# Performance work log

Measured on AMD Instinct MI355X. Metric: run time of the kernel, lower is better.

The kernel has to match this reference:

```python
import jax, jax.numpy as jnp
import numpy as np

N = 20000   # atoms
E = 320000  # edges (avg degree 16)
H = 128     # hidden_channels / num_filters
G = 128     # num_gaussians
L = 4       # num_interactions
B = 200     # molecules
V = 80      # _MAX_ATOM_TYPE
CUT = 5.0
LOG2 = float(np.log(2.0))


def setup_inputs() -> dict:
    key = jax.random.key(0)
    ks = jax.random.split(key, 20)
    s = 0.05
    pos = jax.random.uniform(ks[0], (N, 3), dtype=jnp.float32) * 2.5  # dists < 5 = cutoff
    z = jax.random.randint(ks[1], (N,), 0, V)
    batch = jnp.sort(jax.random.randint(ks[2], (N,), 0, B))
    row = jax.random.randint(ks[3], (E,), 0, N)
    off = jax.random.randint(ks[4], (E,), 1, N)
    col = (row + off) % N  # guarantee row != col (no zero distances)
    edge_index = jnp.stack([row, col], axis=0)
    return {
        'pos': pos, 'z': z, 'batch': batch, 'edge_index': edge_index,
        'emb': jax.random.normal(ks[5], (V, H), jnp.float32) * s,
        'mlp_w1': jax.random.normal(ks[6], (L, G, H), jnp.float32) * s,
        'mlp_b1': jnp.zeros((L, H), jnp.float32),
        'mlp_w2': jax.random.normal(ks[7], (L, H, H), jnp.float32) * s,
        'mlp_b2': jnp.zeros((L, H), jnp.float32),
        'conv_lin1_w': jax.random.normal(ks[8], (L, H, H), jnp.float32) * s,
        'conv_lin2_w': jax.random.normal(ks[9], (L, H, H), jnp.float32) * s,
        'conv_lin2_b': jnp.zeros((L, H), jnp.float32),
        'blk_lin_w': jax.random.normal(ks[10], (L, H, H), jnp.float32) * s,
        'blk_lin_b': jnp.zeros((L, H), jnp.float32),
        'head_w1': jax.random.normal(ks[11], (H, H // 2), jnp.float32) * s,
        'head_b1': jnp.zeros((H // 2,), jnp.float32),
        'head_w2': jax.random.normal(ks[12], (H // 2, 1), jnp.float32) * s,
        'head_b2': jnp.zeros((1,), jnp.float32),
    }


def _ssp(x):  # ShiftedSoftplus
    return jax.nn.softplus(x) - LOG2


def _energy(pos, emb, mlp_w1, mlp_b1, mlp_w2, mlp_b2, conv_lin1_w, conv_lin2_w,
            conv_lin2_b, blk_lin_w, blk_lin_b, head_w1, head_b1, head_w2, head_b2,
            z, batch, edge_index):
    row, col = edge_index[0], edge_index[1]
    diff = pos[row] - pos[col]
    d = jnp.sqrt(jnp.sum(diff * diff, axis=-1))  # [E]
    # GaussianSmearing(0, cutoff, G)
    offset = jnp.linspace(0.0, CUT, G, dtype=pos.dtype)
    coeff = -0.5 / (offset[1] - offset[0]) ** 2
    edge_attr = jnp.exp(coeff * (d[:, None] - offset[None, :]) ** 2)  # [E,G]
    Ccut = 0.5 * (jnp.cos(d * jnp.pi / CUT) + 1.0)  # [E]
    h = emb[z]  # [N,H]
    for i in range(L):
        # per-edge filter MLP * cosine cutoff
        W = _ssp(edge_attr @ mlp_w1[i] + mlp_b1[i]) @ mlp_w2[i] + mlp_b2[i]
        W = W * Ccut[:, None]  # [E,H]
        hx = h @ conv_lin1_w[i]  # lin1, no bias
        msg = hx[row] * W  # gather x_j * filter
        agg = jax.ops.segment_sum(msg, col, num_segments=N)  # scatter-add
        v = agg @ conv_lin2_w[i] + conv_lin2_b[i]
        h = h + (_ssp(v) @ blk_lin_w[i] + blk_lin_b[i])  # residual InteractionBlock
    hh = _ssp(h @ head_w1 + head_b1) @ head_w2 + head_b2  # [N,1]
    return jax.ops.segment_sum(hh[:, 0], batch, num_segments=B)  # [B]


def reference(pos, z, batch, edge_index, emb, mlp_w1, mlp_b1, mlp_w2, mlp_b2,
              conv_lin1_w, conv_lin2_w, conv_lin2_b, blk_lin_w, blk_lin_b,
              head_w1, head_b1, head_w2, head_b2):
    args = (emb, mlp_w1, mlp_b1, mlp_w2, mlp_b2, conv_lin1_w, conv_lin2_w,
            conv_lin2_b, blk_lin_w, blk_lin_b, head_w1, head_b1, head_w2, head_b2)
    out = _energy(pos, *args, z, batch, edge_index)
    # forces = -d(sum(energy))/d(pos), matching torch.autograd.grad with ones grad_outputs
    forces = -jax.grad(lambda p: jnp.sum(_energy(p, *args, z, batch, edge_index)))(pos)
    return out, forces
```

## Files before the change

kernel.cpp:

```cpp
#include <hip/hip_runtime.h>

#define HD 128

constexpr int N_ATOMS = 20000;
constexpr int N_EDGES = 320000;
constexpr int NLAY   = 4;
constexpr int NMOL   = 200;
constexpr float FCUT  = 5.0f;
constexpr float DELTA = FCUT / 127.0f;
constexpr float GCOEFF = -0.5f / (DELTA * DELTA);
constexpr float PI_F  = 3.14159265358979323846f;
constexpr float LN2F  = 0.6931471805599453f;

typedef unsigned short u16;
typedef __attribute__((ext_vector_type(8))) short short8v;
typedef __attribute__((ext_vector_type(4))) float f32x4;

__device__ __forceinline__ float sspf(float x) {
  return fmaxf(x, 0.0f) + log1pf(expf(-fabsf(x))) - LN2F;
}
__device__ __forceinline__ float sigmf(float x) {
  return 1.0f / (1.0f + expf(-x));
}

__device__ __forceinline__ unsigned bfpack(float a, float b) {
  unsigned ua = __float_as_uint(a);
  unsigned ub = __float_as_uint(b);
  ua = (ua + 0x7FFFu + ((ua >> 16) & 1u)) >> 16;
  ub = (ub + 0x7FFFu + ((ub >> 16) & 1u)) >> 16;
  return (ub << 16) | ua;
}
__device__ __forceinline__ float bflo(unsigned p) { return __uint_as_float(p << 16); }
__device__ __forceinline__ float bfhi(unsigned p) { return __uint_as_float(p & 0xFFFF0000u); }
__device__ __forceinline__ u16 f2bf(float x) {
  unsigned u = __float_as_uint(x);
  u = (u + 0x7FFFu + ((u >> 16) & 1u)) >> 16;
  return (u16)u;
}
__device__ __forceinline__ float bf2f(u16 b) { return __uint_as_float((unsigned)b << 16); }

__device__ __forceinline__ unsigned packhl(float s) {
  unsigned hs = __float_as_uint(s) & 0xffff0000u;
  float lo = s - __uint_as_float(hs);
  return hs | (__float_as_uint(lo) >> 16);
}

__device__ __forceinline__ unsigned hpair_f32(unsigned a, unsigned b, unsigned& lopair) {
  unsigned ha = a & 0xffff0000u, hb = b & 0xffff0000u;
  float la = __uint_as_float(a) - __uint_as_float(ha);
  float lb = __uint_as_float(b) - __uint_as_float(hb);
  lopair = (__float_as_uint(lb) & 0xffff0000u) | (__float_as_uint(la) >> 16);
  return hb | (ha >> 16);
}


__global__ __launch_bounds__(256) void h0_k(
    const float* __restrict__ emb, const int* __restrict__ z,
    float* __restrict__ h0)
{
  int i = blockIdx.x * 256 + threadIdx.x;
  if (i >= N_ATOMS * HD) return;
  int n = i >> 7, k = i & 127;
  h0[i] = emb[z[n] * HD + k];
}

__global__ __launch_bounds__(256) void wprep_k(
    const float* __restrict__ l1, const float* __restrict__ l2,
    const float* __restrict__ bw, const float* __restrict__ mw1,
    const float* __restrict__ mw2,
    u16* __restrict__ wt, u16* __restrict__ wp, u16* __restrict__ mt)
{
  int i = blockIdx.x * 256 + threadIdx.x;
  if (i >= NLAY * 5 * HD * HD) return;
  int e = i & (HD * HD - 1);
  int wl = i >> 14;
  int wsel = wl % 5;
  int lay = wl / 5;
  const float* W;
  if      (wsel == 0) W = l1;
  else if (wsel == 1) W = l2;
  else if (wsel == 2) W = bw;
  else if (wsel == 3) W = mw1;
  else                W = mw2;
  W += (size_t)lay * HD * HD;
  u16 b = f2bf(W[e]);
  int k = e >> 7, n = e & 127;
  if (wsel < 3) {
    size_t base = (size_t)(lay * 3 + wsel) << 14;
    wp[base + e] = b;
    wt[base + (size_t)n * HD + k] = b;
  } else {
    size_t base = (size_t)(lay * 2 + (wsel - 3)) << 14;
    mt[base + (size_t)n * HD + k] = b;
  }
}

__global__ __launch_bounds__(256) void histboth_k(
    const int* __restrict__ row, const int* __restrict__ col,
    int* __restrict__ cntR, int* __restrict__ cntC)
{
  int e = blockIdx.x * 256 + threadIdx.x;
  if (e >= N_EDGES) return;
  atomicAdd(&cntC[col[e]], 1);
  atomicAdd(&cntR[row[e]], 1);
}

__global__ __launch_bounds__(256) void scan2_k(
    const int* __restrict__ cnt0, const int* __restrict__ cnt1,
    int* __restrict__ cptr, int* __restrict__ rptr,
    int* __restrict__ cur0, int* __restrict__ cur1,
    int* __restrict__ binc, int* __restrict__ binr)
{
  constexpr int CH = 80;
  __shared__ int part[256];
  __shared__ int lh[256];
  const int* cnt = blockIdx.x == 0 ? cnt0 : cnt1;
  int* ptr = blockIdx.x == 0 ? cptr : rptr;
  int* cur = blockIdx.x == 0 ? cur0 : cur1;
  int* bin = blockIdx.x == 0 ? binc : binr;
  int t = threadIdx.x;
  lh[t] = 0;
  int base = t * CH;
  int v[CH];
  if (base + CH <= N_ATOMS) {
#pragma unroll
    for (int i = 0; i < CH / 4; i++) {
      int4 q = *(const int4*)(cnt + base + i * 4);
      v[4*i+0] = q.x; v[4*i+1] = q.y; v[4*i+2] = q.z; v[4*i+3] = q.w;
    }
  } else {
#pragma unroll
    for (int i = 0; i < CH; i++)
      v[i] = (base + i < N_ATOMS) ? cnt[base + i] : 0;
  }
  __syncthreads();
#pragma unroll
  for (int i = 0; i < CH; i++)
    if (base + i < N_ATOMS) atomicAdd(&lh[255 - min(v[i], 255)], 1);
  int s = 0;
#pragma unroll
  for (int i = 0; i < CH; i++) s += v[i];
  part[t] = s;
  __syncthreads();
  bin[t] = lh[t];
  for (int off = 1; off < 256; off <<= 1) {
    int u = (t >= off) ? part[t - off] : 0;
    __syncthreads();
    part[t] += u;
    __syncthreads();
  }
  int run = part[t] - s;
#pragma unroll
  for (int i = 0; i < CH; i++) {
    int idx = base + i;
    if (idx < N_ATOMS) { ptr[idx] = run; cur[idx] = run; }
    else if (idx == N_ATOMS) ptr[idx] = run;
    run += v[i];
  }
}

__global__ __launch_bounds__(256) void scatboth_k(
    const float* __restrict__ pos, const int* __restrict__ row,
    const int* __restrict__ col, int* __restrict__ cur0,
    int* __restrict__ cur1, uint2* __restrict__ cpk2,
    uint2* __restrict__ rpk2, float* __restrict__ cdist,
    float* __restrict__ rdist, int* __restrict__ cslot, float inv_h)
{
  int e = blockIdx.x * 256 + threadIdx.x;
  if (e >= N_EDGES) return;
  int r = row[e], c = col[e];
  float dx = pos[3*r+0] - pos[3*c+0];
  float dy = pos[3*r+1] - pos[3*c+1];
  float dz = pos[3*r+2] - pos[3*c+2];
  float d = sqrtf(dx*dx + dy*dy + dz*dz);
  float fi = d * inv_h;
  int i0 = (int)fi;
  float t = fi - (float)i0;
  unsigned pk = (unsigned)c | ((unsigned)i0 << 16);
  unsigned tu = __float_as_uint(t);
  int pr = atomicAdd(&cur1[r], 1);
  rpk2[pr] = make_uint2(pk, tu);
  rdist[pr] = d;
  int pc = atomicAdd(&cur0[c], 1);
  cpk2[pc] = make_uint2((unsigned)r | ((unsigned)i0 << 16), tu);
  cdist[pc] = d;
  cslot[pc] = pr;
}

__global__ __launch_bounds__(256) void dscan_k(
    int* __restrict__ binc, int* __restrict__ binr)
{
  int* bin = blockIdx.x == 0 ? binc : binr;
  __shared__ int sh[256];
  int t = threadIdx.x;
  int v = bin[t];
  sh[t] = v;
  __syncthreads();
  for (int off = 1; off < 256; off <<= 1) {
    int u = (t >= off) ? sh[t - off] : 0;
    __syncthreads();
    sh[t] += u;
    __syncthreads();
  }
  bin[t] = sh[t] - v;
}

__global__ __launch_bounds__(256) void dscat_k(
    const int* __restrict__ cptr, const int* __restrict__ rptr,
    int* __restrict__ binc, int* __restrict__ binr,
    int* __restrict__ permc, int* __restrict__ permr)
{
  __shared__ int lhc[256], lhr[256], lbc[256], lbr[256];
  int t = threadIdx.x;
  lhc[t] = 0; lhr[t] = 0;
  __syncthreads();
  int a = blockIdx.x * 256 + t;
  int bc = 0, br = 0, rc = 0, rr = 0;
  bool valid = a < N_ATOMS;
  if (valid) {
    int dc = cptr[a+1] - cptr[a];
    int dr = rptr[a+1] - rptr[a];
    bc = 255 - min(dc, 255);
    br = 255 - min(dr, 255);
    rc = atomicAdd(&lhc[bc], 1);
    rr = atomicAdd(&lhr[br], 1);
  }
  __syncthreads();
  if (lhc[t] > 0) lbc[t] = atomicAdd(&binc[t], lhc[t]);
  if (lhr[t] > 0) lbr[t] = atomicAdd(&binr[t], lhr[t]);
  __syncthreads();
  if (valid) {
    permc[lbc[bc] + rc] = a;
    permr[lbr[br] + rr] = a;
  }
}

__global__ __launch_bounds__(256) void nodeA_k(
    float* __restrict__ A, float* __restrict__ dA, int nnode, float hstep)
{
  int i = blockIdx.x * 256 + threadIdx.x;
  if (i >= nnode * HD) return;
  int node = i >> 7, g = i & 127;
  float d = (float)node * hstep;
  float t = d - (float)g * DELTA;
  float a = expf(GCOEFF * t * t);
  A[i] = a;
  dA[i] = a * 2.0f * GCOEFF * t;
}

__global__ __launch_bounds__(256) void nodeact_k(
    const float* __restrict__ t1, const float* __restrict__ u,
    float* __restrict__ s, float* __restrict__ sp, int total)
{
  int i = blockIdx.x * 256 + threadIdx.x;
  if (i >= total) return;
  float x = t1[i];
  s[i] = sspf(x);
  sp[i] = sigmf(x) * u[i];
}

__global__ __launch_bounds__(256) void nodecomb_k(
    const float* __restrict__ P0, const float* __restrict__ D0,
    unsigned* __restrict__ T, int nnode, float hstep)
{
  int i = blockIdx.x * 256 + threadIdx.x;
  int total = NLAY * nnode * HD;
  if (i >= total) return;
  int rem = i % (nnode * HD);
  int node = rem >> 7;
  float d = (float)node * hstep;
  float C  = 0.5f * cosf(d * (PI_F / FCUT)) + 0.5f;
  float Cp = -0.5f * sinf(d * (PI_F / FCUT)) * (PI_F / FCUT);
  float p = P0[i], q = D0[i];
  T[i] = bfpack(p * C, q * C + p * Cp);
}

__device__ __forceinline__ void wave_mm(
    const float* __restrict__ Av, const u16* __restrict__ Bt,
    int m0, int wbase, int lc, int lg, int mclamp, f32x4 acc[2])
{
  short8v bfr[4][2];
#pragma unroll
  for (int ks = 0; ks < 4; ++ks)
#pragma unroll
    for (int nt = 0; nt < 2; ++nt)
      bfr[ks][nt] = *(const short8v*)(Bt + (size_t)(wbase + nt*16 + lc) * HD + ks*32 + lg*8);
  int ar = m0 + lc;
  if (ar > mclamp) ar = mclamp;
  f32x4 z = {0.f, 0.f, 0.f, 0.f};
  acc[0] = z; acc[1] = z;
#pragma unroll
  for (int ks = 0; ks < 4; ++ks) {
    const float* p = Av + (size_t)ar * HD + ks*32 + lg*8;
    uint4 u0 = *(const uint4*)p;
    uint4 u1 = *(const uint4*)(p + 4);
    unsigned p0l, p1l, p2l, p3l;
    unsigned p0h = hpair_f32(u0.x, u0.y, p0l);
    unsigned p1h = hpair_f32(u0.z, u0.w, p1l);
    unsigned p2h = hpair_f32(u1.x, u1.y, p2l);
    unsigned p3h = hpair_f32(u1.z, u1.w, p3l);
    uint4 hv = make_uint4(p0h, p1h, p2h, p3h);
    uint4 lv = make_uint4(p0l, p1l, p2l, p3l);
    short8v ah = *(short8v*)&hv, al = *(short8v*)&lv;
    acc[0] = __builtin_amdgcn_mfma_f32_16x16x32_bf16(ah, bfr[ks][0], acc[0], 0, 0, 0);
    acc[1] = __builtin_amdgcn_mfma_f32_16x16x32_bf16(ah, bfr[ks][1], acc[1], 0, 0, 0);
    acc[0] = __builtin_amdgcn_mfma_f32_16x16x32_bf16(al, bfr[ks][0], acc[0], 0, 0, 0);
    acc[1] = __builtin_amdgcn_mfma_f32_16x16x32_bf16(al, bfr[ks][1], acc[1], 0, 0, 0);
  }
}

__device__ __forceinline__ void wave_mm_lds(
    const unsigned (*__restrict__ Sl)[132], const u16* __restrict__ Bt,
    int wbase, int lc, int lg, f32x4 acc[2])
{
  short8v bfr[4][2];
#pragma unroll
  for (int ks = 0; ks < 4; ++ks)
#pragma unroll
    for (int nt = 0; nt < 2; ++nt)
      bfr[ks][nt] = *(const short8v*)(Bt + (size_t)(wbase + nt*16 + lc) * HD + ks*32 + lg*8);
  f32x4 z = {0.f, 0.f, 0.f, 0.f};
  acc[0] = z; acc[1] = z;
#pragma unroll
  for (int ks = 0; ks < 4; ++ks) {
    uint4 u0 = *(const uint4*)&Sl[lc][ks*32 + lg*8];
    uint4 u1 = *(const uint4*)&Sl[lc][ks*32 + lg*8 + 4];
    uint4 hv = make_uint4(
      (u0.y & 0xffff0000u) | (u0.x >> 16),
      (u0.w & 0xffff0000u) | (u0.z >> 16),
      (u1.y & 0xffff0000u) | (u1.x >> 16),
      (u1.w & 0xffff0000u) | (u1.z >> 16));
    uint4 lv = make_uint4(
      (u0.y << 16) | (u0.x & 0xffffu),
      (u0.w << 16) | (u0.z & 0xffffu),
      (u1.y << 16) | (u1.x & 0xffffu),
      (u1.w << 16) | (u1.z & 0xffffu));
    short8v ah = *(short8v*)&hv, al = *(short8v*)&lv;
    acc[0] = __builtin_amdgcn_mfma_f32_16x16x32_bf16(ah, bfr[ks][0], acc[0], 0, 0, 0);
    acc[1] = __builtin_amdgcn_mfma_f32_16x16x32_bf16(ah, bfr[ks][1], acc[1], 0, 0, 0);
    acc[0] = __builtin_amdgcn_mfma_f32_16x16x32_bf16(al, bfr[ks][0], acc[0], 0, 0, 0);
    acc[1] = __builtin_amdgcn_mfma_f32_16x16x32_bf16(al, bfr[ks][1], acc[1], 0, 0, 0);
  }
}

__global__ __launch_bounds__(256) void nmm_hx_k(
    const float* __restrict__ h, const u16* __restrict__ Bt,
    u16* __restrict__ hx, int M)
{
  int t = threadIdx.x, lane = t & 63;
  int lc = lane & 15, lg = lane >> 4;
  int wbase = (t >> 6) * 32;
  int m0 = blockIdx.x * 16;
  f32x4 acc[2];
  wave_mm(h, Bt, m0, wbase, lc, lg, M - 1, acc);
#pragma unroll
  for (int nt = 0; nt < 2; ++nt) {
    int ccol = wbase + nt*16 + lc;
#pragma unroll
    for (int j = 0; j < 4; ++j) {
      int grow = m0 + lg*4 + j;
      if (grow < M) hx[(size_t)grow * HD + ccol] = f2bf(acc[nt][j]);
    }
  }
}

__global__ __launch_bounds__(256) void ftail_f_k(
    const float* __restrict__ agg, const u16* __restrict__ l2t,
    const float* __restrict__ l2b, const u16* __restrict__ bwt,
    const float* __restrict__ bb, const float* __restrict__ h,
    u16* __restrict__ svb, float* __restrict__ hout,
    const u16* __restrict__ l1n, u16* __restrict__ hxn, int M)
{
  __shared__ unsigned Sl[16][132];
  int t = threadIdx.x, lane = t & 63;
  int lc = lane & 15, lg = lane >> 4;
  int wbase = (t >> 6) * 32;
  int m0 = blockIdx.x * 16;
  f32x4 acc[2];
  wave_mm(agg, l2t, m0, wbase, lc, lg, M - 1, acc);
#pragma unroll
  for (int nt = 0; nt < 2; ++nt) {
    int ccol = wbase + nt*16 + lc;
    float bv = l2b[ccol];
#pragma unroll
    for (int j = 0; j < 4; ++j) {
      int lrow = lg*4 + j;
      int grow = m0 + lrow;
      float s = 0.0f;
      if (grow < M) {
        float x = acc[nt][j] + bv;
        svb[(size_t)grow * HD + ccol] = f2bf(sigmf(x));
        s = sspf(x);
      }
      Sl[lrow][ccol] = packhl(s);
    }
  }
  __syncthreads();
  wave_mm_lds(Sl, bwt, wbase, lc, lg, acc);

  float ho[2][4];
#pragma unroll
  for (int nt = 0; nt < 2; ++nt) {
    int ccol = wbase + nt*16 + lc;
    float bv = bb[ccol];
#pragma unroll
    for (int j = 0; j < 4; ++j) {
      int grow = m0 + lg*4 + j;
      float x = 0.0f;
      if (grow < M) {
        x = acc[nt][j] + bv + h[(size_t)grow * HD + ccol];
        hout[(size_t)grow * HD + ccol] = x;
      }
      ho[nt][j] = x;
    }
  }
  if (l1n) {
    __syncthreads();
#pragma unroll
    for (int nt = 0; nt < 2; ++nt) {
      int ccol = wbase + nt*16 + lc;
#pragma unroll
      for (int j = 0; j < 4; ++j)
        Sl[lg*4 + j][ccol] = packhl(ho[nt][j]);
    }
    __syncthreads();
    wave_mm_lds(Sl, l1n, wbase, lc, lg, acc);
#pragma unroll
    for (int nt = 0; nt < 2; ++nt) {
      int ccol = wbase + nt*16 + lc;
#pragma unroll
      for (int j = 0; j < 4; ++j) {
        int grow = m0 + lg*4 + j;
        if (grow < M) hxn[(size_t)grow * HD + ccol] = f2bf(acc[nt][j]);
      }
    }
  }
}

__global__ __launch_bounds__(256) void bhead2_f_k(
    const float* __restrict__ aggprev, const u16* __restrict__ l1prev,
    const float* __restrict__ gadd, const float* __restrict__ gdirect,
    const u16* __restrict__ bwp, const u16* __restrict__ svb,
    const u16* __restrict__ l2p, u16* __restrict__ dagg,
    float* __restrict__ gout, int M)
{
  __shared__ unsigned Sl[16][132];
  int t = threadIdx.x, lane = t & 63;
  int lc = lane & 15, lg = lane >> 4;
  int wbase = (t >> 6) * 32;
  int m0 = blockIdx.x * 16;
  f32x4 acc[2];
  if (aggprev) {
    wave_mm(aggprev, l1prev, m0, wbase, lc, lg, M - 1, acc);
#pragma unroll
    for (int nt = 0; nt < 2; ++nt) {
      int ccol = wbase + nt*16 + lc;
#pragma unroll
      for (int j = 0; j < 4; ++j) {
        int lrow = lg*4 + j;
        int grow = m0 + lrow;
        float x = 0.0f;
        if (grow < M) {
          x = acc[nt][j] + gadd[(size_t)grow * HD + ccol];
          if (gout) gout[(size_t)grow * HD + ccol] = x;
        }
        Sl[lrow][ccol] = packhl(x);
      }
    }
    __syncthreads();
    wave_mm_lds(Sl, bwp, wbase, lc, lg, acc);
    __syncthreads();
  } else {
    wave_mm(gdirect, bwp, m0, wbase, lc, lg, M - 1, acc);
  }
#pragma unroll
  for (int nt = 0; nt < 2; ++nt) {
    int ccol = wbase + nt*16 + lc;
#pragma unroll
    for (int j = 0; j < 4; ++j) {
      int lrow = lg*4 + j;
      int grow = m0 + lrow;
      float dv = 0.0f;
      if (grow < M)
        dv = acc[nt][j] * bf2f(svb[(size_t)grow * HD + ccol]);
      Sl[lrow][ccol] = packhl(dv);
    }
  }
  __syncthreads();
  wave_mm_lds(Sl, l2p, wbase, lc, lg, acc);
#pragma unroll
  for (int nt = 0; nt < 2; ++nt) {
    int ccol = wbase + nt*16 + lc;
#pragma unroll
    for (int j = 0; j < 4; ++j) {
      int grow = m0 + lg*4 + j;
      if (grow < M) dagg[(size_t)grow * HD + ccol] = f2bf(acc[nt][j]);
    }
  }
}

__global__ __launch_bounds__(256) void tblmm2_k(
    const float* __restrict__ A0, const float* __restrict__ A1, size_t astride,
    const u16* __restrict__ Bt, size_t bstride,
    const float* __restrict__ bias0, size_t biasstride,
    float* __restrict__ C0, float* __restrict__ C1, size_t cstride, int M)
{
  int l = blockIdx.y;
  int zz = blockIdx.z;
  const float* A = (zz ? A1 : A0) + (size_t)l * astride;
  const u16* B = Bt + (size_t)l * bstride;
  const float* bias = zz ? nullptr : (bias0 ? bias0 + (size_t)l * biasstride : nullptr);
  float* C = (zz ? C1 : C0) + (size_t)l * cstride;
  int t = threadIdx.x, lane = t & 63;
  int lc = lane & 15, lg = lane >> 4;
  int wbase = (t >> 6) * 32;
  int m0 = blockIdx.x * 16;
  f32x4 acc[2];
  wave_mm(A, B, m0, wbase, lc, lg, M - 1, acc);
#pragma unroll
  for (int nt = 0; nt < 2; ++nt) {
    int ccol = wbase + nt*16 + lc;
    float bv = bias ? bias[ccol] : 0.0f;
#pragma unroll
    for (int j = 0; j < 4; ++j) {
      int grow = m0 + lg*4 + j;
      if (grow < M) C[(size_t)grow * HD + ccol] = acc[nt][j] + bv;
    }
  }
}

__global__ __launch_bounds__(256) void gath_fwd_k(
    const int* __restrict__ perm, const int* __restrict__ cptr,
    const uint2* __restrict__ cpk2, const unsigned* __restrict__ T,
    const unsigned* __restrict__ hx, float* __restrict__ agg, float hstep)
{
  int ai = blockIdx.x * 4 + (threadIdx.x >> 6);
  if (ai >= N_ATOMS) return;
  int a = perm[ai];
  int half = (threadIdx.x >> 5) & 1;
  int l32 = threadIdx.x & 31;
  int ch = l32 * 4;
  int beg = cptr[a], end = cptr[a + 1];
  float s0 = 0.f, s1 = 0.f, s2 = 0.f, s3 = 0.f;
#pragma unroll 2
  for (int j = beg + half; j < end; j += 2) {
    uint2 pk2 = cpk2[j];
    float t = __uint_as_float(pk2.y);
    int other = pk2.x & 0xffffu;
    float t2 = t * t, t3 = t2 * t;
    float cx = 2.f*t3 - 3.f*t2 + 1.f;
    float cy = (t3 - 2.f*t2 + t) * hstep;
    float cz = 3.f*t2 - 2.f*t3;
    float cw = (t3 - t2) * hstep;
    const unsigned* tp = T + (size_t)(pk2.x >> 16) * HD + ch;
    uint4 q0 = *(const uint4*)(tp);
    uint4 q1 = *(const uint4*)(tp + HD);
    uint2 hp = *(const uint2*)(hx + (size_t)other * 64 + l32 * 2);
    float v0 = cx*bflo(q0.x) + cy*bfhi(q0.x) + cz*bflo(q1.x) + cw*bfhi(q1.x);
    float v1 = cx*bflo(q0.y) + cy*bfhi(q0.y) + cz*bflo(q1.y) + cw*bfhi(q1.y);
    float v2 = cx*bflo(q0.z) + cy*bfhi(q0.z) + cz*bflo(q1.z) + cw*bfhi(q1.z);
    float v3 = cx*bflo(q0.w) + cy*bfhi(q0.w) + cz*bflo(q1.w) + cw*bfhi(q1.w);
    s0 = fmaf(bflo(hp.x), v0, s0);
    s1 = fmaf(bfhi(hp.x), v1, s1);
    s2 = fmaf(bflo(hp.y), v2, s2);
    s3 = fmaf(bfhi(hp.y), v3, s3);
  }
  s0 += __shfl_xor(s0, 32, 64);
  s1 += __shfl_xor(s1, 32, 64);
  s2 += __shfl_xor(s2, 32, 64);
  s3 += __shfl_xor(s3, 32, 64);
  if (half == 0)
    *(float4*)(agg + (size_t)a * HD + ch) = make_float4(s0, s1, s2, s3);
}

__global__ __launch_bounds__(256) void gath_bwd_k(
    const int* __restrict__ perm, const int* __restrict__ rptr,
    const uint2* __restrict__ rpk2, const unsigned* __restrict__ T,
    const unsigned* __restrict__ dagg, const unsigned* __restrict__ hx,
    float* __restrict__ dhx, float* __restrict__ ddslot, int accum,
    int need_dhx, float hstep, float inv_h)
{
  int ai = blockIdx.x * 4 + (threadIdx.x >> 6);
  if (ai >= N_ATOMS) return;
  int a = perm[ai];
  int half = (threadIdx.x >> 5) & 1;
  int l32 = threadIdx.x & 31;
  int ch = l32 * 4;
  int beg = rptr[a], end = rptr[a + 1];
  uint2 hp = *(const uint2*)(hx + (size_t)a * 64 + l32 * 2);
  float h0 = bflo(hp.x), h1 = bfhi(hp.x), h2 = bflo(hp.y), h3 = bfhi(hp.y);
  float s0 = 0.f, s1 = 0.f, s2 = 0.f, s3 = 0.f;
#pragma unroll 2
  for (int j = beg + half; j < end; j += 2) {
    uint2 pk2 = rpk2[j];
    float t = __uint_as_float(pk2.y);
    int other = pk2.x & 0xffffu;
    float t2 = t * t, t3 = t2 * t;
    float cbx = (6.f*t2 - 6.f*t) * inv_h;
    float cby = 3.f*t2 - 4.f*t + 1.f;
    float cbz = -cbx;
    float cbw = 3.f*t2 - 2.f*t;
    const unsigned* tp = T + (size_t)(pk2.x >> 16) * HD + ch;
    uint4 q0 = *(const uint4*)(tp);
    uint4 q1 = *(const uint4*)(tp + HD);
    uint2 dp = *(const uint2*)(dagg + (size_t)other * 64 + l32 * 2);
    float da0 = bflo(dp.x), da1 = bfhi(dp.x), da2 = bflo(dp.y), da3 = bfhi(dp.y);
    float x0l = bflo(q0.x), x0h = bfhi(q0.x), y0l = bflo(q1.x), y0h = bfhi(q1.x);
    float x1l = bflo(q0.y), x1h = bfhi(q0.y), y1l = bflo(q1.y), y1h = bfhi(q1.y);
    float x2l = bflo(q0.z), x2h = bfhi(q0.z), y2l = bflo(q1.z), y2h = bfhi(q1.z);
    float x3l = bflo(q0.w), x3h = bfhi(q0.w), y3l = bflo(q1.w), y3h = bfhi(q1.w);
    float g0 = cbx*x0l + cby*x0h + cbz*y0l + cbw*y0h;
    float g1 = cbx*x1l + cby*x1h + cbz*y1l + cbw*y1h;
    float g2 = cbx*x2l + cby*x2h + cbz*y2l + cbw*y2h;
    float g3 = cbx*x3l + cby*x3h + cbz*y3l + cbw*y3h;
    float dah0 = da0*h0, dah1 = da1*h1, dah2 = da2*h2, dah3 = da3*h3;
    float dot = dah0*g0;
    dot = fmaf(dah1, g1, dot);
    dot = fmaf(dah2, g2, dot);
    dot = fmaf(dah3, g3, dot);
#pragma unroll
    for (int off = 16; off > 0; off >>= 1) dot += __shfl_down(dot, off, 32);
    if (l32 == 0) ddslot[j] = accum ? (ddslot[j] + dot) : dot;
    if (need_dhx) {
      float cax = 2.f*t3 - 3.f*t2 + 1.f;
      float cay = (t3 - 2.f*t2 + t) * hstep;
      float caz = 3.f*t2 - 2.f*t3;
      float caw = (t3 - t2) * hstep;
      float v0 = cax*x0l + cay*x0h + caz*y0l + caw*y0h;
      float v1 = cax*x1l + cay*x1h + caz*y1l + caw*y1h;
      float v2 = cax*x2l + cay*x2h + caz*y2l + caw*y2h;
      float v3 = cax*x3l + cay*x3h + caz*y3l + caw*y3h;
      s0 = fmaf(da0, v0, s0);
      s1 = fmaf(da1, v1, s1);
      s2 = fmaf(da2, v2, s2);
      s3 = fmaf(da3, v3, s3);
    }
  }
  if (need_dhx) {
    s0 += __shfl_xor(s0, 32, 64);
    s1 += __shfl_xor(s1, 32, 64);
    s2 += __shfl_xor(s2, 32, 64);
    s3 += __shfl_xor(s3, 32, 64);
    if (half == 0)
      *(float4*)(dhx + (size_t)a * HD + ch) = make_float4(s0, s1, s2, s3);
  }
}

__global__ __launch_bounds__(256) void headf_k(
    const float* __restrict__ h4, const float* __restrict__ hw1,
    const float* __restrict__ hb1, const float* __restrict__ hw2,
    const float* __restrict__ hb2, float* __restrict__ ea,
    float* __restrict__ gh)
{
  __shared__ float As[16][68];
  __shared__ float Bs[16][132];
  __shared__ float Ss[64][68];
  __shared__ float red[64][17];
  int t = threadIdx.x;
  int tx = t & 15, ty = t >> 4;
  int m0 = blockIdx.x * 64;

  float acc4[4][4];
#pragma unroll
  for (int r = 0; r < 4; r++)
#pragma unroll
    for (int c = 0; c < 4; c++) acc4[r][c] = 0.0f;

  for (int k0 = 0; k0 < HD; k0 += 16) {
    {
      int rrow = t >> 2;
      int kg = (t & 3) * 4;
      int gm = m0 + rrow;
      float4 av = make_float4(0.f, 0.f, 0.f, 0.f);
      if (gm < N_ATOMS) av = *(const float4*)(h4 + (size_t)gm * HD + k0 + kg);
      As[kg+0][rrow] = av.x; As[kg+1][rrow] = av.y;
      As[kg+2][rrow] = av.z; As[kg+3][rrow] = av.w;
    }
    if (t < 256) {
      int kk = t >> 4;
      int n4 = (t & 15) * 4;
      float4 bv = *(const float4*)(hw1 + (size_t)(k0 + kk) * 64 + n4);
      *(float4*)&Bs[kk][n4] = bv;
    }
    __syncthreads();
#pragma unroll
    for (int kk = 0; kk < 16; kk++) {
      float a[4], b[4];
#pragma unroll
      for (int r = 0; r < 4; r++) a[r] = As[kk][ty * 4 + r];
#pragma unroll
      for (int c = 0; c < 4; c++) b[c] = Bs[kk][tx * 4 + c];
#pragma unroll
      for (int r = 0; r < 4; r++)
#pragma unroll
        for (int c = 0; c < 4; c++) acc4[r][c] = fmaf(a[r], b[c], acc4[r][c]);
    }
    __syncthreads();
  }

  {
    int n0 = tx * 4;
    float b1v[4], w2v[4];
#pragma unroll
    for (int c = 0; c < 4; c++) { b1v[c] = hb1[n0 + c]; w2v[c] = hw2[n0 + c]; }
#pragma unroll
    for (int r = 0; r < 4; r++) {
      int lr = ty * 4 + r;
      float p = 0.0f;
#pragma unroll
      for (int c = 0; c < 4; c++) {
        float x = acc4[r][c] + b1v[c];
        p += sspf(x) * w2v[c];
        Ss[lr][n0 + c] = sigmf(x) * w2v[c];
      }
      red[lr][tx] = p;
    }
  }
  __syncthreads();
  if (t < 64) {
    int gm = m0 + t;
    if (gm < N_ATOMS) {
      float s = hb2[0];
#pragma unroll
      for (int j = 0; j < 16; j++) s += red[t][j];
      ea[gm] = s;
    }
  }

  float acc[4][8];
#pragma unroll
  for (int r = 0; r < 4; r++)
#pragma unroll
    for (int c = 0; c < 8; c++) acc[r][c] = 0.0f;

  for (int j0 = 0; j0 < 64; j0 += 16) {
#pragma unroll
    for (int it = 0; it < 2; it++) {
      int idx = t + it * 256;
      int n = idx >> 2;
      int jg = (idx & 3) * 4;
      float4 bv = *(const float4*)(hw1 + (size_t)n * 64 + j0 + jg);
      Bs[jg+0][n] = bv.x; Bs[jg+1][n] = bv.y;
      Bs[jg+2][n] = bv.z; Bs[jg+3][n] = bv.w;
    }
    __syncthreads();
#pragma unroll
    for (int kk = 0; kk < 16; kk++) {
      float a[4], b[8];
#pragma unroll
      for (int r = 0; r < 4; r++) a[r] = Ss[ty * 4 + r][j0 + kk];
#pragma unroll
      for (int c = 0; c < 8; c++) b[c] = Bs[kk][tx * 8 + c];
#pragma unroll
      for (int r = 0; r < 4; r++)
#pragma unroll
        for (int c = 0; c < 8; c++) acc[r][c] = fmaf(a[r], b[c], acc[r][c]);
    }
    __syncthreads();
  }

  int n0 = tx * 8;
#pragma unroll
  for (int r = 0; r < 4; r++) {
    int gm = m0 + ty * 4 + r;
    if (gm >= N_ATOMS) continue;
    *(float4*)(gh + (size_t)gm * HD + n0)     = *(float4*)&acc[r][0];
    *(float4*)(gh + (size_t)gm * HD + n0 + 4) = *(float4*)&acc[r][4];
  }
}

__global__ __launch_bounds__(64) void ered_k(
    const int* __restrict__ batch, const float* __restrict__ ea,
    float* __restrict__ energy)
{
  int m = blockIdx.x;
  int lo = 0, hi = N_ATOMS;
  while (lo < hi) { int mid = (lo + hi) >> 1; if (batch[mid] < m) lo = mid + 1; else hi = mid; }
  int beg = lo;
  lo = beg; hi = N_ATOMS;
  while (lo < hi) { int mid = (lo + hi) >> 1; if (batch[mid] < m + 1) lo = mid + 1; else hi = mid; }
  int end = lo;
  float s = 0.0f;
  for (int i = beg + threadIdx.x; i < end; i += 64) s += ea[i];
#pragma unroll
  for (int off = 32; off > 0; off >>= 1) s += __shfl_down(s, off, 64);
  if (threadIdx.x == 0) energy[m] = s;
}

__global__ __launch_bounds__(256) void forceg_k(
    const int* __restrict__ rptr, const uint2* __restrict__ rpk2,
    const float* __restrict__ rdist,
    const int* __restrict__ cptr, const uint2* __restrict__ cpk2,
    const float* __restrict__ cdist, const int* __restrict__ cslot,
    const float* __restrict__ ddslot, const float* __restrict__ pos,
    float* __restrict__ force)
{
  int idx = blockIdx.x * 256 + threadIdx.x;
  int a = idx >> 3;
  int g = idx & 7;
  if (a >= N_ATOMS) return;
  float px = pos[3*a+0], py = pos[3*a+1], pz = pos[3*a+2];
  float fx = 0.f, fy = 0.f, fz = 0.f;
  int beg = rptr[a], end = rptr[a+1];
  for (int j = beg + g; j < end; j += 8) {
    int o = rpk2[j].x & 0xffffu;
    float w = ddslot[j] / rdist[j];
    fx -= w * (px - pos[3*o+0]);
    fy -= w * (py - pos[3*o+1]);
    fz -= w * (pz - pos[3*o+2]);
  }
  beg = cptr[a]; end = cptr[a+1];
  for (int j = beg + g; j < end; j += 8) {
    int o = cpk2[j].x & 0xffffu;
    float w = ddslot[cslot[j]] / cdist[j];
    fx -= w * (px - pos[3*o+0]);
    fy -= w * (py - pos[3*o+1]);
    fz -= w * (pz - pos[3*o+2]);
  }
#pragma unroll
  for (int off = 4; off > 0; off >>= 1) {
    fx += __shfl_down(fx, off, 8);
    fy += __shfl_down(fy, off, 8);
    fz += __shfl_down(fz, off, 8);
  }
  if (g == 0) {
    force[3*a+0] = fx;
    force[3*a+1] = fy;
    force[3*a+2] = fz;
  }
}

static inline int nblk(int m) { return (m + 63) / 64; }

extern "C" void kernel_launch(void* const* d_in, const int* in_sizes, int n_in,
                              void* d_out, int out_size, void* d_ws, size_t ws_size,
                              hipStream_t stream)
{
  const float* pos   = (const float*)d_in[0];
  const int*   z     = (const int*)d_in[1];
  const int*   batch = (const int*)d_in[2];
  const int*   eidx  = (const int*)d_in[3];
  const float* emb   = (const float*)d_in[4];
  const float* mlp_w1 = (const float*)d_in[5];
  const float* mlp_b1 = (const float*)d_in[6];
  const float* mlp_w2 = (const float*)d_in[7];
  const float* mlp_b2 = (const float*)d_in[8];
  const float* lin1_w = (const float*)d_in[9];
  const float* lin2_w = (const float*)d_in[10];
  const float* lin2_b = (const float*)d_in[11];
  const float* blk_w  = (const float*)d_in[12];
  const float* blk_b  = (const float*)d_in[13];
  const float* hw1 = (const float*)d_in[14];
  const float* hb1 = (const float*)d_in[15];
  const float* hw2 = (const float*)d_in[16];
  const float* hb2 = (const float*)d_in[17];

  float* out = (float*)d_out;
  float* ws  = (float*)d_ws;

  const int* row = eidx;
  const int* col = eidx + N_EDGES;

  const size_t NH = (size_t)N_ATOMS * HD;
  size_t o = 0;
  float* ddslot = ws + o; o += N_EDGES;
  int* cptr = (int*)(ws + o); o += N_ATOMS + 1;
  int* rptr = (int*)(ws + o); o += N_ATOMS + 1;
  int* cnt0 = (int*)(ws + o); o += N_ATOMS;
  int* cnt1 = (int*)(ws + o); o += N_ATOMS;
  int* binc = (int*)(ws + o); o += 256;
  int* binr = (int*)(ws + o); o += 256;
  int* cur0 = (int*)(ws + o); o += N_ATOMS;
  int* cur1 = (int*)(ws + o); o += N_ATOMS;
  int* permc = (int*)(ws + o); o += N_ATOMS;
  int* permr = (int*)(ws + o); o += N_ATOMS;
  int* cslot = (int*)(ws + o); o += N_EDGES;
  float* cdist = ws + o; o += N_EDGES;
  float* rdist = ws + o; o += N_EDGES;
  o = (o + 1) & ~(size_t)1;
  uint2* cpk2 = (uint2*)(ws + o); o += (size_t)2 * N_EDGES;
  uint2* rpk2 = (uint2*)(ws + o); o += (size_t)2 * N_EDGES;
  u16* wt = (u16*)(ws + o); o += (size_t)NLAY * 3 * HD * HD / 2;
  u16* wp = (u16*)(ws + o); o += (size_t)NLAY * 3 * HD * HD / 2;
  u16* mt = (u16*)(ws + o); o += (size_t)NLAY * 2 * HD * HD / 2;
  float* hxb[4];
  for (int i = 0; i < 4; i++) { hxb[i] = ws + o; o += NH / 2; }
  float* svb[4];
  for (int i = 0; i < 4; i++) { svb[i] = ws + o; o += NH / 2; }
  float* hA  = ws + o; o += NH;
  float* hB  = ws + o; o += NH;
  float* agg = ws + o; o += NH;
  float* g0b = ws + o; o += NH;
  float* g1b = ws + o; o += NH;
  float* dgb = ws + o; o += NH / 2;

  int NT = 1024;
  while (NT > 128) {
    size_t need = o + (size_t)NLAY * (NT + 1) * HD;
    if (need * sizeof(float) <= ws_size) break;
    NT >>= 1;
  }
  const int NN = NT + 1;
  const float hstep = FCUT / (float)NT;
  const float inv_h = (float)NT / FCUT;
  unsigned* T = (unsigned*)(ws + o); o += (size_t)NLAY * NN * HD;

  const int EB = (N_EDGES + 255) / 256;
  const int ABK = (N_ATOMS + 255) / 256;

  hipMemsetAsync(cnt0, 0, 2 * N_ATOMS * sizeof(int), stream);

  wprep_k<<<(NLAY * 5 * HD * HD + 255) / 256, 256, 0, stream>>>(
      lin1_w, lin2_w, blk_w, mlp_w1, mlp_w2, wt, wp, mt);

  histboth_k<<<EB, 256, 0, stream>>>(row, col, cnt1, cnt0);
  scan2_k<<<2, 256, 0, stream>>>(cnt0, cnt1, cptr, rptr, cur0, cur1, binc, binr);
  scatboth_k<<<EB, 256, 0, stream>>>(pos, row, col, cur0, cur1, cpk2, rpk2,
                                     cdist, rdist, cslot, inv_h);

  dscan_k<<<2, 256, 0, stream>>>(binc, binr);
  dscat_k<<<ABK, 256, 0, stream>>>(cptr, rptr, binc, binr, permc, permr);

  {
    const size_t LNH = (size_t)NN * HD;
    float* Anode  = agg;
    float* dAnode = agg + LNH;
    float* t1 = dgb;
    float* u  = g0b;
    float* s  = g1b;
    float* sp = hA;
    nodeA_k<<<((int)LNH + 255) / 256, 256, 0, stream>>>(Anode, dAnode, NN, hstep);
    dim3 gB16((NN + 15) / 16, NLAY, 2);
    tblmm2_k<<<gB16, 256, 0, stream>>>(Anode, dAnode, 0, mt, 32768,
                                       mlp_b1, HD, t1, u, LNH, NN);
    int tot = (int)(NLAY * LNH);
    nodeact_k<<<(tot + 255) / 256, 256, 0, stream>>>(t1, u, s, sp, tot);
    float* P0 = dgb;
    float* D0 = g0b;
    tblmm2_k<<<gB16, 256, 0, stream>>>(s, sp, LNH, mt + 16384, 32768,
                                       mlp_b2, HD, P0, D0, LNH, NN);
    nodecomb_k<<<(tot + 255) / 256, 256, 0, stream>>>(P0, D0, T, NN, hstep);
  }

  h0_k<<<(N_ATOMS * HD + 255) / 256, 256, 0, stream>>>(emb, z, hA);

  const int AB = (N_ATOMS + 3) / 4;
  const int GB = nblk(N_ATOMS);
  const int NB16 = (N_ATOMS + 15) / 16;

  float* hcur = hA;
  float* hnxt = hB;
  nmm_hx_k<<<NB16, 256, 0, stream>>>(hcur, wt, (u16*)hxb[0], N_ATOMS);
  for (int i = 0; i < NLAY; i++) {
    const u16* l2t = wt + ((size_t)(i*3 + 1) << 14);
    const u16* bwt = wt + ((size_t)(i*3 + 2) << 14);
    const u16* l1n = (i < NLAY - 1) ? wt + ((size_t)((i+1)*3 + 0) << 14) : nullptr;
    u16* hxn = (i < NLAY - 1) ? (u16*)hxb[i+1] : nullptr;
    const float* l2bi = lin2_b + (size_t)i * HD;
    const float* bbi  = blk_b + (size_t)i * HD;
    const unsigned* Tl = T + (size_t)i * NN * HD;

    gath_fwd_k<<<AB, 256, 0, stream>>>(permc, cptr, cpk2, Tl,
                                       (const unsigned*)hxb[i], agg, hstep);
    ftail_f_k<<<NB16, 256, 0, stream>>>(agg, l2t, l2bi, bwt, bbi, hcur,
                                        (u16*)svb[i], hnxt, l1n, hxn, N_ATOMS);
    float* tmp = hcur; hcur = hnxt; hnxt = tmp;
  }

  float* ea = dgb;
  headf_k<<<GB, 256, 0, stream>>>(hcur, hw1, hb1, hw2, hb2, ea, g0b);
  ered_k<<<NMOL, 64, 0, stream>>>(batch, ea, out);

  float* gcur = g0b;
  float* gnxt = g1b;
  for (int i = NLAY - 1; i >= 0; i--) {
    const u16* l2p = wp + ((size_t)(i*3 + 1) << 14);
    const u16* bwp = wp + ((size_t)(i*3 + 2) << 14);
    const unsigned* Tl = T + (size_t)i * NN * HD;

    if (i == NLAY - 1) {
      bhead2_f_k<<<NB16, 256, 0, stream>>>(nullptr, nullptr, nullptr, gcur,
                                           bwp, (const u16*)svb[i], l2p,
                                           (u16*)dgb, nullptr, N_ATOMS);
    } else {
      const u16* l1nx = wp + ((size_t)((i+1)*3 + 0) << 14);
      float* gout = (i > 0) ? gnxt : nullptr;
      bhead2_f_k<<<NB16, 256, 0, stream>>>(agg, l1nx, gcur, nullptr,
                                           bwp, (const u16*)svb[i], l2p,
                                           (u16*)dgb, gout, N_ATOMS);
      if (i > 0) { float* tmp = gcur; gcur = gnxt; gnxt = tmp; }
    }
    gath_bwd_k<<<AB, 256, 0, stream>>>(permr, rptr, rpk2, Tl,
                                       (const unsigned*)dgb,
                                       (const unsigned*)hxb[i], agg, ddslot,
                                       i != NLAY - 1, i != 0, hstep, inv_h);
  }

  forceg_k<<<(N_ATOMS * 8 + 255) / 256, 256, 0, stream>>>(
      rptr, rpk2, rdist, cptr, cpk2, cdist, cslot, ddslot, pos, out + NMOL);
}
```

Before: 763.3 us.

## Widen per-lane channels in edge gather kernels and recompute distances from packed keys

The forward and backward edge-gather kernels now have each wavefront handle four edges at a time, with 16 lanes each covering 8 channels through 16-byte loads, instead of two edges with 32 lanes each covering 4 channels. This is meant to raise memory-level parallelism and reduce per-edge shuffle reduction depth. Separately, the per-edge distance arrays are removed: the force kernel rebuilds the distance from the packed table index and fraction, saving the writes and reads of two edge-sized arrays. The rebuilt distance carries small rounding error, and the wider lanes raise register pressure.

```diff
diff --git a/kernel.cpp b/kernel.cpp
--- a/kernel.cpp
+++ b/kernel.cpp
@@ -163,8 +163,7 @@
     const float* __restrict__ pos, const int* __restrict__ row,
     const int* __restrict__ col, int* __restrict__ cur0,
     int* __restrict__ cur1, uint2* __restrict__ cpk2,
-    uint2* __restrict__ rpk2, float* __restrict__ cdist,
-    float* __restrict__ rdist, int* __restrict__ cslot, float inv_h)
+    uint2* __restrict__ rpk2, int* __restrict__ cslot, float inv_h)
 {
   int e = blockIdx.x * 256 + threadIdx.x;
   if (e >= N_EDGES) return;
@@ -180,10 +179,8 @@
   unsigned tu = __float_as_uint(t);
   int pr = atomicAdd(&cur1[r], 1);
   rpk2[pr] = make_uint2(pk, tu);
-  rdist[pr] = d;
   int pc = atomicAdd(&cur0[c], 1);
   cpk2[pc] = make_uint2((unsigned)r | ((unsigned)i0 << 16), tu);
-  cdist[pc] = d;
   cslot[pc] = pr;
 }
 
@@ -537,13 +534,15 @@
   int ai = blockIdx.x * 4 + (threadIdx.x >> 6);
   if (ai >= N_ATOMS) return;
   int a = perm[ai];
-  int half = (threadIdx.x >> 5) & 1;
-  int l32 = threadIdx.x & 31;
-  int ch = l32 * 4;
+  int lane = threadIdx.x & 63;
+  int grp = lane >> 4;
+  int l16 = lane & 15;
+  int ch = l16 * 8;
   int beg = cptr[a], end = cptr[a + 1];
-  float s0 = 0.f, s1 = 0.f, s2 = 0.f, s3 = 0.f;
-#pragma unroll 2
-  for (int j = beg + half; j < end; j += 2) {
+  float s[8];
+#pragma unroll
+  for (int c = 0; c < 8; c++) s[c] = 0.f;
+  for (int j = beg + grp; j < end; j += 4) {
     uint2 pk2 = cpk2[j];
     float t = __uint_as_float(pk2.y);
     int other = pk2.x & 0xffffu;
@@ -553,24 +552,30 @@
     float cz = 3.f*t2 - 2.f*t3;
     float cw = (t3 - t2) * hstep;
     const unsigned* tp = T + (size_t)(pk2.x >> 16) * HD + ch;
-    uint4 q0 = *(const uint4*)(tp);
-    uint4 q1 = *(const uint4*)(tp + HD);
-    uint2 hp = *(const uint2*)(hx + (size_t)other * 64 + l32 * 2);
-    float v0 = cx*bflo(q0.x) + cy*bfhi(q0.x) + cz*bflo(q1.x) + cw*bfhi(q1.x);
-    float v1 = cx*bflo(q0.y) + cy*bfhi(q0.y) + cz*bflo(q1.y) + cw*bfhi(q1.y);
-    float v2 = cx*bflo(q0.z) + cy*bfhi(q0.z) + cz*bflo(q1.z) + cw*bfhi(q1.z);
-    float v3 = cx*bflo(q0.w) + cy*bfhi(q0.w) + cz*bflo(q1.w) + cw*bfhi(q1.w);
-    s0 = fmaf(bflo(hp.x), v0, s0);
-    s1 = fmaf(bfhi(hp.x), v1, s1);
-    s2 = fmaf(bflo(hp.y), v2, s2);
-    s3 = fmaf(bfhi(hp.y), v3, s3);
-  }
-  s0 += __shfl_xor(s0, 32, 64);
-  s1 += __shfl_xor(s1, 32, 64);
-  s2 += __shfl_xor(s2, 32, 64);
-  s3 += __shfl_xor(s3, 32, 64);
-  if (half == 0)
-    *(float4*)(agg + (size_t)a * HD + ch) = make_float4(s0, s1, s2, s3);
+    uint4 q0a = *(const uint4*)(tp);
+    uint4 q0b = *(const uint4*)(tp + 4);
+    uint4 q1a = *(const uint4*)(tp + HD);
+    uint4 q1b = *(const uint4*)(tp + HD + 4);
+    uint4 hp = *(const uint4*)(hx + (size_t)other * 64 + l16 * 4);
+    unsigned q0[8] = {q0a.x, q0a.y, q0a.z, q0a.w, q0b.x, q0b.y, q0b.z, q0b.w};
+    unsigned q1[8] = {q1a.x, q1a.y, q1a.z, q1a.w, q1b.x, q1b.y, q1b.z, q1b.w};
+    unsigned hh[4] = {hp.x, hp.y, hp.z, hp.w};
+#pragma unroll
+    for (int c = 0; c < 8; c++) {
+      float v = cx*bflo(q0[c]) + cy*bfhi(q0[c]) + cz*bflo(q1[c]) + cw*bfhi(q1[c]);
+      float hv = (c & 1) ? bfhi(hh[c >> 1]) : bflo(hh[c >> 1]);
+      s[c] = fmaf(hv, v, s[c]);
+    }
+  }
+#pragma unroll
+  for (int c = 0; c < 8; c++) {
+    s[c] += __shfl_xor(s[c], 16, 64);
+    s[c] += __shfl_xor(s[c], 32, 64);
+  }
+  if (grp == 0) {
+    *(float4*)(agg + (size_t)a * HD + ch)     = make_float4(s[0], s[1], s[2], s[3]);
+    *(float4*)(agg + (size_t)a * HD + ch + 4) = make_float4(s[4], s[5], s[6], s[7]);
+  }
 }
 
 __global__ __launch_bounds__(256) void gath_bwd_k(
@@ -583,15 +588,21 @@
   int ai = blockIdx.x * 4 + (threadIdx.x >> 6);
   if (ai >= N_ATOMS) return;
   int a = perm[ai];
-  int half = (threadIdx.x >> 5) & 1;
-  int l32 = threadIdx.x & 31;
-  int ch = l32 * 4;
+  int lane = threadIdx.x & 63;
+  int grp = lane >> 4;
+  int l16 = lane & 15;
+  int ch = l16 * 8;
   int beg = rptr[a], end = rptr[a + 1];
-  uint2 hp = *(const uint2*)(hx + (size_t)a * 64 + l32 * 2);
-  float h0 = bflo(hp.x), h1 = bfhi(hp.x), h2 = bflo(hp.y), h3 = bfhi(hp.y);
-  float s0 = 0.f, s1 = 0.f, s2 = 0.f, s3 = 0.f;
-#pragma unroll 2
-  for (int j = beg + half; j < end; j += 2) {
+  uint4 hp = *(const uint4*)(hx + (size_t)a * 64 + l16 * 4);
+  unsigned hhw[4] = {hp.x, hp.y, hp.z, hp.w};
+  float hv[8];
+#pragma unroll
+  for (int c = 0; c < 8; c++)
+    hv[c] = (c & 1) ? bfhi(hhw[c >> 1]) : bflo(hhw[c >> 1]);
+  float s[8];
+#pragma unroll
+  for (int c = 0; c < 8; c++) s[c] = 0.f;
+  for (int j = beg + grp; j < end; j += 4) {
     uint2 pk2 = rpk2[j];
     float t = __uint_as_float(pk2.y);
     int other = pk2.x & 0xffffu;
@@ -601,48 +612,43 @@
     float cbz = -cbx;
     float cbw = 3.f*t2 - 2.f*t;
     const unsigned* tp = T + (size_t)(pk2.x >> 16) * HD + ch;
-    uint4 q0 = *(const uint4*)(tp);
-    uint4 q1 = *(const uint4*)(tp + HD);
-    uint2 dp = *(const uint2*)(dagg + (size_t)other * 64 + l32 * 2);
-    float da0 = bflo(dp.x), da1 = bfhi(dp.x), da2 = bflo(dp.y), da3 = bfhi(dp.y);
-    float x0l = bflo(q0.x), x0h = bfhi(q0.x), y0l = bflo(q1.x), y0h = bfhi(q1.x);
-    float x1l = bflo(q0.y), x1h = bfhi(q0.y), y1l = bflo(q1.y), y1h = bfhi(q1.y);
-    float x2l = bflo(q0.z), x2h = bfhi(q0.z), y2l = bflo(q1.z), y2h = bfhi(q1.z);
-    float x3l = bflo(q0.w), x3h = bfhi(q0.w), y3l = bflo(q1.w), y3h = bfhi(q1.w);
-    float g0 = cbx*x0l + cby*x0h + cbz*y0l + cbw*y0h;
-    float g1 = cbx*x1l + cby*x1h + cbz*y1l + cbw*y1h;
-    float g2 = cbx*x2l + cby*x2h + cbz*y2l + cbw*y2h;
-    float g3 = cbx*x3l + cby*x3h + cbz*y3l + cbw*y3h;
-    float dah0 = da0*h0, dah1 = da1*h1, dah2 = da2*h2, dah3 = da3*h3;
-    float dot = dah0*g0;
-    dot = fmaf(dah1, g1, dot);
-    dot = fmaf(dah2, g2, dot);
-    dot = fmaf(dah3, g3, dot);
-#pragma unroll
-    for (int off = 16; off > 0; off >>= 1) dot += __shfl_down(dot, off, 32);
-    if (l32 == 0) ddslot[j] = accum ? (ddslot[j] + dot) : dot;
-    if (need_dhx) {
-      float cax = 2.f*t3 - 3.f*t2 + 1.f;
-      float cay = (t3 - 2.f*t2 + t) * hstep;
-      float caz = 3.f*t2 - 2.f*t3;
-      float caw = (t3 - t2) * hstep;
-      float v0 = cax*x0l + cay*x0h + caz*y0l + caw*y0h;
-      float v1 = cax*x1l + cay*x1h + caz*y1l + caw*y1h;
-      float v2 = cax*x2l + cay*x2h + caz*y2l + caw*y2h;
-      float v3 = cax*x3l + cay*x3h + caz*y3l + caw*y3h;
-      s0 = fmaf(da0, v0, s0);
-      s1 = fmaf(da1, v1, s1);
-      s2 = fmaf(da2, v2, s2);
-      s3 = fmaf(da3, v3, s3);
-    }
+    uint4 q0a = *(const uint4*)(tp);
+    uint4 q0b = *(const uint4*)(tp + 4);
+    uint4 q1a = *(const uint4*)(tp + HD);
+    uint4 q1b = *(const uint4*)(tp + HD + 4);
+    uint4 dp = *(const uint4*)(dagg + (size_t)other * 64 + l16 * 4);
+    unsigned q0[8] = {q0a.x, q0a.y, q0a.z, q0a.w, q0b.x, q0b.y, q0b.z, q0b.w};
+    unsigned q1[8] = {q1a.x, q1a.y, q1a.z, q1a.w, q1b.x, q1b.y, q1b.z, q1b.w};
+    unsigned dw[4] = {dp.x, dp.y, dp.z, dp.w};
+    float dot = 0.f;
+#pragma unroll
+    for (int c = 0; c < 8; c++) {
+      float da = (c & 1) ? bfhi(dw[c >> 1]) : bflo(dw[c >> 1]);
+      float g = cbx*bflo(q0[c]) + cby*bfhi(q0[c]) + cbz*bflo(q1[c]) + cbw*bfhi(q1[c]);
+      dot = fmaf(da * hv[c], g, dot);
+      if (need_dhx) {
+        float cax = 2.f*t3 - 3.f*t2 + 1.f;
+        float cay = (t3 - 2.f*t2 + t) * hstep;
+        float caz = 3.f*t2 - 2.f*t3;
+        float caw = (t3 - t2) * hstep;
+        float v = cax*bflo(q0[c]) + cay*bfhi(q0[c]) + caz*bflo(q1[c]) + caw*bfhi(q1[c]);
+        s[c] = fmaf(da, v, s[c]);
+      }
+    }
+#pragma unroll
+    for (int off = 8; off > 0; off >>= 1) dot += __shfl_down(dot, off, 16);
+    if (l16 == 0) ddslot[j] = accum ? (ddslot[j] + dot) : dot;
   }
   if (need_dhx) {
-    s0 += __shfl_xor(s0, 32, 64);
-    s1 += __shfl_xor(s1, 32, 64);
-    s2 += __shfl_xor(s2, 32, 64);
-    s3 += __shfl_xor(s3, 32, 64);
-    if (half == 0)
-      *(float4*)(dhx + (size_t)a * HD + ch) = make_float4(s0, s1, s2, s3);
+#pragma unroll
+    for (int c = 0; c < 8; c++) {
+      s[c] += __shfl_xor(s[c], 16, 64);
+      s[c] += __shfl_xor(s[c], 32, 64);
+    }
+    if (grp == 0) {
+      *(float4*)(dhx + (size_t)a * HD + ch)     = make_float4(s[0], s[1], s[2], s[3]);
+      *(float4*)(dhx + (size_t)a * HD + ch + 4) = make_float4(s[4], s[5], s[6], s[7]);
+    }
   }
 }
 
@@ -789,11 +795,9 @@
 
 __global__ __launch_bounds__(256) void forceg_k(
     const int* __restrict__ rptr, const uint2* __restrict__ rpk2,
-    const float* __restrict__ rdist,
     const int* __restrict__ cptr, const uint2* __restrict__ cpk2,
-    const float* __restrict__ cdist, const int* __restrict__ cslot,
-    const float* __restrict__ ddslot, const float* __restrict__ pos,
-    float* __restrict__ force)
+    const int* __restrict__ cslot, const float* __restrict__ ddslot,
+    const float* __restrict__ pos, float* __restrict__ force, float hstep)
 {
   int idx = blockIdx.x * 256 + threadIdx.x;
   int a = idx >> 3;
@@ -803,16 +807,20 @@
   float fx = 0.f, fy = 0.f, fz = 0.f;
   int beg = rptr[a], end = rptr[a+1];
   for (int j = beg + g; j < end; j += 8) {
-    int o = rpk2[j].x & 0xffffu;
-    float w = ddslot[j] / rdist[j];
+    uint2 p = rpk2[j];
+    int o = p.x & 0xffffu;
+    float d = ((float)(p.x >> 16) + __uint_as_float(p.y)) * hstep;
+    float w = ddslot[j] / d;
     fx -= w * (px - pos[3*o+0]);
     fy -= w * (py - pos[3*o+1]);
     fz -= w * (pz - pos[3*o+2]);
   }
   beg = cptr[a]; end = cptr[a+1];
   for (int j = beg + g; j < end; j += 8) {
-    int o = cpk2[j].x & 0xffffu;
-    float w = ddslot[cslot[j]] / cdist[j];
+    uint2 p = cpk2[j];
+    int o = p.x & 0xffffu;
+    float d = ((float)(p.x >> 16) + __uint_as_float(p.y)) * hstep;
+    float w = ddslot[cslot[j]] / d;
     fx -= w * (px - pos[3*o+0]);
     fy -= w * (py - pos[3*o+1]);
     fz -= w * (pz - pos[3*o+2]);
@@ -875,8 +883,6 @@
   int* permc = (int*)(ws + o); o += N_ATOMS;
   int* permr = (int*)(ws + o); o += N_ATOMS;
   int* cslot = (int*)(ws + o); o += N_EDGES;
-  float* cdist = ws + o; o += N_EDGES;
-  float* rdist = ws + o; o += N_EDGES;
   o = (o + 1) & ~(size_t)1;
   uint2* cpk2 = (uint2*)(ws + o); o += (size_t)2 * N_EDGES;
   uint2* rpk2 = (uint2*)(ws + o); o += (size_t)2 * N_EDGES;
@@ -916,7 +922,7 @@
   histboth_k<<<EB, 256, 0, stream>>>(row, col, cnt1, cnt0);
   scan2_k<<<2, 256, 0, stream>>>(cnt0, cnt1, cptr, rptr, cur0, cur1, binc, binr);
   scatboth_k<<<EB, 256, 0, stream>>>(pos, row, col, cur0, cur1, cpk2, rpk2,
-                                     cdist, rdist, cslot, inv_h);
+                                     cslot, inv_h);
 
   dscan_k<<<2, 256, 0, stream>>>(binc, binr);
   dscat_k<<<ABK, 256, 0, stream>>>(cptr, rptr, binc, binr, permc, permr);
@@ -997,5 +1003,5 @@
   }
 
   forceg_k<<<(N_ATOMS * 8 + 255) / 256, 256, 0, stream>>>(
-      rptr, rpk2, rdist, cptr, cpk2, cdist, cslot, ddslot, pos, out + NMOL);
-}
+      rptr, rpk2, cptr, cpk2, cslot, ddslot, pos, out + NMOL, hstep);
+}
```

Result: slower. 787.0 us (+3.1%).
